# Optimization experiments

Measured on AMD Instinct MI355X. Metric: run time of the kernel, lower is better.

## Reference

```python
import jax, jax.numpy as jnp
from jax import lax
import numpy as np

B, TQ, T = 64, 2, 2048
HID, ENC, U, FILT, K = 1024, 512, 256, 32, 31


def setup_inputs() -> dict:
    key = jax.random.key(0)
    ks = jax.random.split(key, 12)
    def w(k, shape, fan_in):
        return jax.random.normal(k, shape, jnp.float32) / np.sqrt(fan_in)
    return {
        "query": jax.random.normal(ks[0], (B, TQ, HID), jnp.float32),
        "state": jax.random.uniform(ks[1], (B, T), jnp.float32),
        "memory": jax.random.normal(ks[2], (B, T, ENC), jnp.float32),
        "Wq": w(ks[3], (HID, U), HID), "bq": jnp.zeros((U,), jnp.float32),
        "Wm": w(ks[4], (ENC, U), ENC), "bm": jnp.zeros((U,), jnp.float32),
        "Wl": w(ks[5], (FILT, U), FILT), "bl": jnp.zeros((U,), jnp.float32),
        "conv_w": w(ks[6], (FILT, 1, K), K), "conv_b": jnp.zeros((FILT,), jnp.float32),
        "We": w(ks[7], (U, U), U), "be": jnp.zeros((U,), jnp.float32),
        "v_a": w(ks[8], (U,), U),
    }


def reference(query, state, memory, Wq, bq, Wm, bm, Wl, bl, conv_w, conv_b, We, be, v_a):
    # memory projection (done in `initialize` in the original): [B,T,U]
    mem_proj = jnp.einsum("bte,eu->btu", memory, Wm) + bm
    # query projection then slice timestep 1 -> [B,1,U]
    pq = (jnp.einsum("bqh,hu->bqu", query, Wq) + bq)[:, 1:2, :]
    # location features: 1-D conv over time of previous alignment, 'same' padding
    x = state[:, None, :]                                    # [B,1,T]
    f = lax.conv_general_dilated(x, conv_w, (1,), "SAME",
                                 dimension_numbers=("NCH", "OIH", "NCH"))
    f = f + conv_b[None, :, None]                            # [B,FILT,T]
    loc = jnp.einsum("bft,fu->btu", f, Wl) + bl              # [B,T,U]
    # additive energy with tanh, reduced against v_a -> [B,T]
    h = jnp.tanh(jnp.einsum("btu,uv->btv", pq + loc + mem_proj, We) + be)
    energy = jnp.einsum("btu,u->bt", h, v_a)
    # smoothing normalization: sigmoid / sum(sigmoid)
    s = jax.nn.sigmoid(energy)
    alignment = s / jnp.sum(s, axis=-1, keepdims=True)
    # cumulate_weights=True: accumulate onto previous alignment
    cum_alignment = state + alignment
    # context against projected memory: [B,1,U]
    context = jnp.einsum("bt,btu->bu", cum_alignment, mem_proj)[:, None, :]
    return context
```

## Files before the change

### kernel.cpp

```cpp
#include <hip/hip_runtime.h>
#include <hip/hip_bf16.h>
#include <math.h>

#define Bq 64
#define Tt 2048
#define TQn 2
#define HIDn 1024
#define ENCn 512
#define Un 256
#define FILTn 32
#define KKn 31

#define TTILE 32
#define NCHUNK (Tt / TTILE)
#define LDK 520

typedef short short8 __attribute__((ext_vector_type(8)));
typedef float f32x4  __attribute__((ext_vector_type(4)));
typedef unsigned short ushort_t;
typedef unsigned int   uint_t;

union S8 { short8 v; uint_t u[4]; };

__device__ __forceinline__ ushort_t f2b(float f) {
    union { float f; uint_t u; } x; x.f = f;
    uint_t r = x.u + 0x7fffu + ((x.u >> 16) & 1u);
    return (ushort_t)(r >> 16);
}
__device__ __forceinline__ uint_t cvt_pk(float lo, float hi) {
    union { __hip_bfloat162 h; uint_t u; } x;
    x.h = __float22bfloat162_rn(make_float2(lo, hi));
    return x.u;
}
__device__ __forceinline__ float b2f(uint_t u16) {
    union { uint_t i; float f; } x; x.i = u16 << 16;
    return x.f;
}
__device__ __forceinline__ float tanh_fast(float x) {
    const float e = __expf(2.0f * x);
    return 1.0f - 2.0f * __builtin_amdgcn_rcpf(e + 1.0f);
}

__global__ void k_prep1(const float* __restrict__ We, const float* __restrict__ Wm,
                        const float* __restrict__ Wl, const float* __restrict__ conv_w,
                        const float* __restrict__ bq, const float* __restrict__ bm,
                        const float* __restrict__ bl, const float* __restrict__ conv_b,
                        ushort_t* __restrict__ WmWeT, ushort_t* __restrict__ CWT,
                        float* __restrict__ cvec)
{
    const int blk = blockIdx.x;
    const int v = threadIdx.x;
    if (blk < 512) {
        const int e = blk;
        float a0 = 0.f, a1 = 0.f, a2 = 0.f, a3 = 0.f;
        #pragma unroll 4
        for (int u = 0; u < Un; u += 4) {
            a0 += Wm[(size_t)e * Un + u + 0] * We[(u + 0) * Un + v];
            a1 += Wm[(size_t)e * Un + u + 1] * We[(u + 1) * Un + v];
            a2 += Wm[(size_t)e * Un + u + 2] * We[(u + 2) * Un + v];
            a3 += Wm[(size_t)e * Un + u + 3] * We[(u + 3) * Un + v];
        }
        WmWeT[(size_t)v * ENCn + e] = f2b((a0 + a1) + (a2 + a3));
    } else if (blk < 516) {
        const int vc = (blk - 512) * 64;
        __shared__ float wlwe[FILTn * 64];
        for (int i = threadIdx.x; i < FILTn * 64; i += 256) {
            const int f = i >> 6, vv = i & 63;
            float a = 0.f;
            #pragma unroll 8
            for (int u = 0; u < Un; ++u) a += Wl[f * Un + u] * We[u * Un + vc + vv];
            wlwe[f * 64 + vv] = a;
        }
        __syncthreads();
        for (int i = threadIdx.x; i < 64 * 32; i += 256) {
            const int vv = i >> 5, k = i & 31;
            float a = 0.f;
            if (k < KKn) {
                #pragma unroll
                for (int f = 0; f < FILTn; ++f) a += conv_w[f * KKn + k] * wlwe[f * 64 + vv];
            }
            CWT[(size_t)(vc + vv) * 32 + k] = f2b(a);
        }
    } else {
        const int u = v;
        float a = bq[u] + bm[u] + bl[u];
        #pragma unroll
        for (int f = 0; f < FILTn; ++f) a += conv_b[f] * Wl[f * Un + u];
        cvec[u] = a;
    }
}

__global__ void k_g(const float* __restrict__ query, const float* __restrict__ Wq,
                    const float* __restrict__ cvec, float* __restrict__ g)
{
    const int b = blockIdx.x, hs = blockIdx.y * 128, u = threadIdx.x;
    const float* q = query + ((size_t)b * TQn + 1) * HIDn + hs;
    float a0 = 0.f, a1 = 0.f, a2 = 0.f, a3 = 0.f;
    #pragma unroll 4
    for (int h = 0; h < 128; h += 4) {
        a0 += q[h + 0] * Wq[(size_t)(hs + h + 0) * Un + u];
        a1 += q[h + 1] * Wq[(size_t)(hs + h + 1) * Un + u];
        a2 += q[h + 2] * Wq[(size_t)(hs + h + 2) * Un + u];
        a3 += q[h + 3] * Wq[(size_t)(hs + h + 3) * Un + u];
    }
    float acc = (a0 + a1) + (a2 + a3);
    if (blockIdx.y == 0) acc += cvec[u];
    atomicAdd(&g[b * Un + u], acc);
}

__global__ void k_zconst(const float* __restrict__ g, const float* __restrict__ We,
                         const float* __restrict__ be, float* __restrict__ zconst)
{
    const int b = blockIdx.x, us = blockIdx.y * 64, v = threadIdx.x;
    float a0 = 0.f, a1 = 0.f;
    #pragma unroll 4
    for (int u = us; u < us + 64; u += 2) {
        a0 += g[b * Un + u]     * We[(size_t)u * Un + v];
        a1 += g[b * Un + u + 1] * We[(size_t)(u + 1) * Un + v];
    }
    float acc = a0 + a1;
    if (blockIdx.y == 0) acc += be[v];
    atomicAdd(&zconst[b * Un + v], acc);
}

__global__ __launch_bounds__(256, 4) void attn_main(
    const float* __restrict__ memory, const float* __restrict__ state,
    const ushort_t* __restrict__ WmWeT, const ushort_t* __restrict__ CWT,
    const float* __restrict__ zconst, const float* __restrict__ v_a,
    float* __restrict__ zA, float* __restrict__ zS,
    float* __restrict__ zSsum, float* __restrict__ zStsum)
{
    const int blk = blockIdx.x;
    const int b  = blk >> 6;
    const int c  = blk & (NCHUNK - 1);
    const int t0 = c * TTILE;
    const int tid = threadIdx.x;

    __shared__ __align__(16) ushort_t mem_s[TTILE * LDK];
    __shared__ __align__(16) float sw_raw[80];
    __shared__ __align__(16) float ep_s[4][TTILE];
    __shared__ __align__(16) float s_s[TTILE];
    float* sw = sw_raw + 1;

    for (int i = tid; i < TTILE + 31; i += 256) {
        const int t = t0 - 15 + i;
        sw[i] = (t >= 0 && t < Tt) ? state[b * Tt + t] : 0.0f;
    }

    const int lane = tid & 63;
    const int w    = tid >> 6;
    const int lm   = lane & 15;
    const int lq   = lane >> 4;
    const int ncol0 = w * 64 + lm;

    const ushort_t* bp0 = WmWeT + (size_t)(ncol0 +  0) * ENCn + lq * 8;
    const ushort_t* bp1 = WmWeT + (size_t)(ncol0 + 16) * ENCn + lq * 8;
    const ushort_t* bp2 = WmWeT + (size_t)(ncol0 + 32) * ENCn + lq * 8;
    const ushort_t* bp3 = WmWeT + (size_t)(ncol0 + 48) * ENCn + lq * 8;

    short8 bbuf[2][4];
    bbuf[0][0] = *(const short8*)(bp0);      bbuf[0][1] = *(const short8*)(bp1);
    bbuf[0][2] = *(const short8*)(bp2);      bbuf[0][3] = *(const short8*)(bp3);
    bbuf[1][0] = *(const short8*)(bp0 + 32); bbuf[1][1] = *(const short8*)(bp1 + 32);
    bbuf[1][2] = *(const short8*)(bp2 + 32); bbuf[1][3] = *(const short8*)(bp3 + 32);

    const float4* memv4 = (const float4*)(memory + ((size_t)b * Tt + t0) * ENCn);
    #pragma unroll
    for (int i = 0; i < 8; ++i) {
        const int idx = i * 256 + tid;
        const int row = idx >> 6;
        const int cw8 = (idx & 63) << 3;
        const float4 m0 = memv4[2 * idx];
        const float4 m1 = memv4[2 * idx + 1];
        S8 v;
        v.u[0] = cvt_pk(m0.x, m0.y); v.u[1] = cvt_pk(m0.z, m0.w);
        v.u[2] = cvt_pk(m1.x, m1.y); v.u[3] = cvt_pk(m1.z, m1.w);
        *(short8*)&mem_s[row * LDK + cw8] = v.v;
    }

    f32x4 acc[2][4] = {};

    __syncthreads();

    const ushort_t* arow0 = &mem_s[(lm) * LDK + lq * 8];
    const ushort_t* arow1 = &mem_s[(16 + lm) * LDK + lq * 8];

    short8 a0c = *(const short8*)(arow0);
    short8 a1c = *(const short8*)(arow1);

    #pragma unroll
    for (int s = 0; s < 16; ++s) {
        const int sa = ((s + 1) & 15) * 32;
        const short8 a0n = *(const short8*)(arow0 + sa);
        const short8 a1n = *(const short8*)(arow1 + sa);
        acc[0][0] = __builtin_amdgcn_mfma_f32_16x16x32_bf16(a0c, bbuf[s & 1][0], acc[0][0], 0, 0, 0);
        acc[0][1] = __builtin_amdgcn_mfma_f32_16x16x32_bf16(a0c, bbuf[s & 1][1], acc[0][1], 0, 0, 0);
        acc[0][2] = __builtin_amdgcn_mfma_f32_16x16x32_bf16(a0c, bbuf[s & 1][2], acc[0][2], 0, 0, 0);
        acc[0][3] = __builtin_amdgcn_mfma_f32_16x16x32_bf16(a0c, bbuf[s & 1][3], acc[0][3], 0, 0, 0);
        acc[1][0] = __builtin_amdgcn_mfma_f32_16x16x32_bf16(a1c, bbuf[s & 1][0], acc[1][0], 0, 0, 0);
        acc[1][1] = __builtin_amdgcn_mfma_f32_16x16x32_bf16(a1c, bbuf[s & 1][1], acc[1][1], 0, 0, 0);
        acc[1][2] = __builtin_amdgcn_mfma_f32_16x16x32_bf16(a1c, bbuf[s & 1][2], acc[1][2], 0, 0, 0);
        acc[1][3] = __builtin_amdgcn_mfma_f32_16x16x32_bf16(a1c, bbuf[s & 1][3], acc[1][3], 0, 0, 0);
        const int sn = ((s + 2) & 15) * 32;
        bbuf[s & 1][0] = *(const short8*)(bp0 + sn);
        bbuf[s & 1][1] = *(const short8*)(bp1 + sn);
        bbuf[s & 1][2] = *(const short8*)(bp2 + sn);
        bbuf[s & 1][3] = *(const short8*)(bp3 + sn);
        a0c = a0n; a1c = a1n;
    }

    {
        S8 ca0, ca1;
        #pragma unroll
        for (int j = 0; j < 4; ++j) {
            const int base0 = lm + lq * 8 + 2 * j;
            ca0.u[j] = cvt_pk(sw[base0],      sw[base0 + 1]);
            ca1.u[j] = cvt_pk(sw[base0 + 16], sw[base0 + 17]);
        }
        const ushort_t* cp = CWT + (size_t)ncol0 * 32 + lq * 8;
        const short8 cb0 = *(const short8*)(cp);
        const short8 cb1 = *(const short8*)(cp + 16 * 32);
        const short8 cb2 = *(const short8*)(cp + 32 * 32);
        const short8 cb3 = *(const short8*)(cp + 48 * 32);
        acc[0][0] = __builtin_amdgcn_mfma_f32_16x16x32_bf16(ca0.v, cb0, acc[0][0], 0, 0, 0);
        acc[0][1] = __builtin_amdgcn_mfma_f32_16x16x32_bf16(ca0.v, cb1, acc[0][1], 0, 0, 0);
        acc[0][2] = __builtin_amdgcn_mfma_f32_16x16x32_bf16(ca0.v, cb2, acc[0][2], 0, 0, 0);
        acc[0][3] = __builtin_amdgcn_mfma_f32_16x16x32_bf16(ca0.v, cb3, acc[0][3], 0, 0, 0);
        acc[1][0] = __builtin_amdgcn_mfma_f32_16x16x32_bf16(ca1.v, cb0, acc[1][0], 0, 0, 0);
        acc[1][1] = __builtin_amdgcn_mfma_f32_16x16x32_bf16(ca1.v, cb1, acc[1][1], 0, 0, 0);
        acc[1][2] = __builtin_amdgcn_mfma_f32_16x16x32_bf16(ca1.v, cb2, acc[1][2], 0, 0, 0);
        acc[1][3] = __builtin_amdgcn_mfma_f32_16x16x32_bf16(ca1.v, cb3, acc[1][3], 0, 0, 0);
    }

    float zc[4], va[4];
    #pragma unroll
    for (int nbi = 0; nbi < 4; ++nbi) {
        const int col = ncol0 + nbi * 16;
        zc[nbi] = zconst[b * Un + col];
        va[nbi] = v_a[col];
    }
    #pragma unroll
    for (int mb = 0; mb < 2; ++mb) {
        #pragma unroll
        for (int r = 0; r < 4; ++r) {
            float ep = 0.f;
            #pragma unroll
            for (int nbi = 0; nbi < 4; ++nbi)
                ep += tanh_fast(acc[mb][nbi][r] + zc[nbi]) * va[nbi];
            ep += __shfl_xor(ep, 1, 64);
            ep += __shfl_xor(ep, 2, 64);
            ep += __shfl_xor(ep, 4, 64);
            ep += __shfl_xor(ep, 8, 64);
            if (lm == 0) ep_s[w][mb * 16 + lq * 4 + r] = ep;
        }
    }
    __syncthreads();

    if (tid < 64) {
        float s = 0.f, st = 0.f;
        if (tid < TTILE) {
            const float energy = ep_s[0][tid] + ep_s[1][tid] + ep_s[2][tid] + ep_s[3][tid];
            s = __builtin_amdgcn_rcpf(1.0f + __expf(-energy));
            s_s[tid] = s;
            st = sw[15 + tid];
        }
        float ssum = s, stsum = st;
        #pragma unroll
        for (int off = 32; off >= 1; off >>= 1) {
            ssum  += __shfl_xor(ssum,  off, 64);
            stsum += __shfl_xor(stsum, off, 64);
        }
        if (tid == 0) {
            atomicAdd(&zSsum[b], ssum);
            atomicAdd(&zStsum[b], stsum);
        }
    }
    __syncthreads();

    const int e0 = tid << 1;
    float aA0 = 0.f, aA1 = 0.f, aS0 = 0.f, aS1 = 0.f;
    #pragma unroll 2
    for (int r4 = 0; r4 < TTILE / 4; ++r4) {
        const float4 sv4 = *(const float4*)&s_s[r4 * 4];
        const float4 st4 = *(const float4*)&sw[15 + r4 * 4];
        const float sv[4] = {sv4.x, sv4.y, sv4.z, sv4.w};
        const float st[4] = {st4.x, st4.y, st4.z, st4.w};
        #pragma unroll
        for (int j = 0; j < 4; ++j) {
            const int r = r4 * 4 + j;
            const uint_t mm = *(const uint_t*)&mem_s[r * LDK + e0];
            const float m0 = b2f(mm & 0xffffu);
            const float m1 = b2f(mm >> 16);
            aA0 += st[j] * m0; aA1 += st[j] * m1;
            aS0 += sv[j] * m0; aS1 += sv[j] * m1;
        }
    }
    atomicAdd(&zA[b * ENCn + e0],     aA0);
    atomicAdd(&zA[b * ENCn + e0 + 1], aA1);
    atomicAdd(&zS[b * ENCn + e0],     aS0);
    atomicAdd(&zS[b * ENCn + e0 + 1], aS1);
}

__global__ void k_final(const float* __restrict__ zA, const float* __restrict__ zS,
                        const float* __restrict__ zSsum, const float* __restrict__ zStsum,
                        const float* __restrict__ Wm, const float* __restrict__ bm,
                        float* __restrict__ out)
{
    const int b = blockIdx.x, e0 = blockIdx.y * 128, u = threadIdx.x;
    const float inv = 1.0f / zSsum[b];
    float a0 = 0.f, a1 = 0.f;
    #pragma unroll 4
    for (int e = e0; e < e0 + 128; e += 2) {
        const float c0 = zA[b * ENCn + e]     + zS[b * ENCn + e]     * inv;
        const float c1 = zA[b * ENCn + e + 1] + zS[b * ENCn + e + 1] * inv;
        a0 += c0 * Wm[(size_t)e * Un + u];
        a1 += c1 * Wm[(size_t)(e + 1) * Un + u];
    }
    float acc = a0 + a1;
    if (blockIdx.y == 0) acc += bm[u] * (zStsum[b] + 1.0f);
    atomicAdd(&out[b * Un + u], acc);
}

extern "C" void kernel_launch(void* const* d_in, const int* in_sizes, int n_in,
                              void* d_out, int out_size, void* d_ws, size_t ws_size,
                              hipStream_t stream)
{
    const float* query  = (const float*)d_in[0];
    const float* state  = (const float*)d_in[1];
    const float* memory = (const float*)d_in[2];
    const float* Wq     = (const float*)d_in[3];
    const float* bq     = (const float*)d_in[4];
    const float* Wm     = (const float*)d_in[5];
    const float* bm     = (const float*)d_in[6];
    const float* Wl     = (const float*)d_in[7];
    const float* bl     = (const float*)d_in[8];
    const float* conv_w = (const float*)d_in[9];
    const float* conv_b = (const float*)d_in[10];
    const float* We     = (const float*)d_in[11];
    const float* be     = (const float*)d_in[12];
    const float* v_a    = (const float*)d_in[13];
    float* out = (float*)d_out;

    float* ws      = (float*)d_ws;
    float* zA      = ws;
    float* zS      = ws + 32768;
    float* zSsum   = ws + 65536;
    float* zStsum  = ws + 65600;
    float* g_      = ws + 65664;
    float* zconst  = ws + 82048;
    float* cvec    = ws + 98432;
    ushort_t* WmWeT = (ushort_t*)(ws + 98688);
    ushort_t* CWT   = (ushort_t*)(ws + 164224);

    hipMemsetAsync(ws, 0, 98432 * sizeof(float), stream);
    hipMemsetAsync(out, 0, (size_t)Bq * Un * sizeof(float), stream);

    hipLaunchKernelGGL(k_prep1, dim3(517), dim3(Un), 0, stream,
                       We, Wm, Wl, conv_w, bq, bm, bl, conv_b, WmWeT, CWT, cvec);
    hipLaunchKernelGGL(k_g, dim3(Bq, 8), dim3(Un), 0, stream, query, Wq, cvec, g_);
    hipLaunchKernelGGL(k_zconst, dim3(Bq, 4), dim3(Un), 0, stream, g_, We, be, zconst);
    hipLaunchKernelGGL(attn_main, dim3(Bq * NCHUNK), dim3(256), 0, stream,
                       memory, state, WmWeT, CWT, zconst, v_a, zA, zS, zSsum, zStsum);
    hipLaunchKernelGGL(k_final, dim3(Bq, 4), dim3(Un), 0, stream,
                       zA, zS, zSsum, zStsum, Wm, bm, out);
}
```

Measured before the change: 557.6 us.

## Process four time chunks per block with register prefetch and MFMA-packed weights

Each attn_main block now loops over four consecutive 32-step time tiles, prefetching the next tile of memory and state into registers while the current tile runs its MFMAs. This cuts the grid by four and amortizes atomics and setup. The WmWe and conv-weight matrices are stored in a fragment-packed layout so each lane reads contiguous 16-byte chunks. The cost is a large register prefetch buffer (launch bounds lowered to 3 blocks) and fewer blocks to spread across CUs.

```diff
diff --git a/kernel.cpp b/kernel.cpp
--- a/kernel.cpp
+++ b/kernel.cpp
@@ -13,6 +13,7 @@
 
 #define TTILE 32
 #define NCHUNK (Tt / TTILE)
+#define NCPB 4
 #define LDK 520
 
 typedef short short8 __attribute__((ext_vector_type(8)));
@@ -41,11 +42,17 @@
     return 1.0f - 2.0f * __builtin_amdgcn_rcpf(e + 1.0f);
 }
 
+__device__ __forceinline__ int bp_idx(int v, int k) {
+    const int seg = (k >> 5) * 16 + (v >> 6) * 4 + ((v >> 4) & 3);
+    const int ln  = ((k >> 3) & 3) * 16 + (v & 15);
+    return seg * 512 + ln * 8 + (k & 7);
+}
+
 __global__ void k_prep1(const float* __restrict__ We, const float* __restrict__ Wm,
                         const float* __restrict__ Wl, const float* __restrict__ conv_w,
                         const float* __restrict__ bq, const float* __restrict__ bm,
                         const float* __restrict__ bl, const float* __restrict__ conv_b,
-                        ushort_t* __restrict__ WmWeT, ushort_t* __restrict__ CWT,
+                        ushort_t* __restrict__ Bp, ushort_t* __restrict__ CWT,
                         float* __restrict__ cvec)
 {
     const int blk = blockIdx.x;
@@ -60,7 +67,7 @@
             a2 += Wm[(size_t)e * Un + u + 2] * We[(u + 2) * Un + v];
             a3 += Wm[(size_t)e * Un + u + 3] * We[(u + 3) * Un + v];
         }
-        WmWeT[(size_t)v * ENCn + e] = f2b((a0 + a1) + (a2 + a3));
+        Bp[bp_idx(v, e)] = f2b((a0 + a1) + (a2 + a3));
     } else if (blk < 516) {
         const int vc = (blk - 512) * 64;
         __shared__ float wlwe[FILTn * 64];
@@ -79,7 +86,7 @@
                 #pragma unroll
                 for (int f = 0; f < FILTn; ++f) a += conv_w[f * KKn + k] * wlwe[f * 64 + vv];
             }
-            CWT[(size_t)(vc + vv) * 32 + k] = f2b(a);
+            CWT[bp_idx(vc + vv, k)] = f2b(a);
         }
     } else {
         const int u = v;
@@ -123,17 +130,16 @@
     atomicAdd(&zconst[b * Un + v], acc);
 }
 
-__global__ __launch_bounds__(256, 4) void attn_main(
+__global__ __launch_bounds__(256, 3) void attn_main(
     const float* __restrict__ memory, const float* __restrict__ state,
-    const ushort_t* __restrict__ WmWeT, const ushort_t* __restrict__ CWT,
+    const ushort_t* __restrict__ Bp, const ushort_t* __restrict__ CWT,
     const float* __restrict__ zconst, const float* __restrict__ v_a,
     float* __restrict__ zA, float* __restrict__ zS,
     float* __restrict__ zSsum, float* __restrict__ zStsum)
 {
     const int blk = blockIdx.x;
-    const int b  = blk >> 6;
-    const int c  = blk & (NCHUNK - 1);
-    const int t0 = c * TTILE;
+    const int b  = blk >> 4;
+    const int cg = blk & 15;
     const int tid = threadIdx.x;
 
     __shared__ __align__(16) ushort_t mem_s[TTILE * LDK];
@@ -142,95 +148,17 @@
     __shared__ __align__(16) float s_s[TTILE];
     float* sw = sw_raw + 1;
 
-    for (int i = tid; i < TTILE + 31; i += 256) {
-        const int t = t0 - 15 + i;
-        sw[i] = (t >= 0 && t < Tt) ? state[b * Tt + t] : 0.0f;
-    }
-
     const int lane = tid & 63;
     const int w    = tid >> 6;
     const int lm   = lane & 15;
     const int lq   = lane >> 4;
     const int ncol0 = w * 64 + lm;
 
-    const ushort_t* bp0 = WmWeT + (size_t)(ncol0 +  0) * ENCn + lq * 8;
-    const ushort_t* bp1 = WmWeT + (size_t)(ncol0 + 16) * ENCn + lq * 8;
-    const ushort_t* bp2 = WmWeT + (size_t)(ncol0 + 32) * ENCn + lq * 8;
-    const ushort_t* bp3 = WmWeT + (size_t)(ncol0 + 48) * ENCn + lq * 8;
-
-    short8 bbuf[2][4];
-    bbuf[0][0] = *(const short8*)(bp0);      bbuf[0][1] = *(const short8*)(bp1);
-    bbuf[0][2] = *(const short8*)(bp2);      bbuf[0][3] = *(const short8*)(bp3);
-    bbuf[1][0] = *(const short8*)(bp0 + 32); bbuf[1][1] = *(const short8*)(bp1 + 32);
-    bbuf[1][2] = *(const short8*)(bp2 + 32); bbuf[1][3] = *(const short8*)(bp3 + 32);
-
-    const float4* memv4 = (const float4*)(memory + ((size_t)b * Tt + t0) * ENCn);
-    #pragma unroll
-    for (int i = 0; i < 8; ++i) {
-        const int idx = i * 256 + tid;
-        const int row = idx >> 6;
-        const int cw8 = (idx & 63) << 3;
-        const float4 m0 = memv4[2 * idx];
-        const float4 m1 = memv4[2 * idx + 1];
-        S8 v;
-        v.u[0] = cvt_pk(m0.x, m0.y); v.u[1] = cvt_pk(m0.z, m0.w);
-        v.u[2] = cvt_pk(m1.x, m1.y); v.u[3] = cvt_pk(m1.z, m1.w);
-        *(short8*)&mem_s[row * LDK + cw8] = v.v;
-    }
-
-    f32x4 acc[2][4] = {};
-
-    __syncthreads();
-
-    const ushort_t* arow0 = &mem_s[(lm) * LDK + lq * 8];
-    const ushort_t* arow1 = &mem_s[(16 + lm) * LDK + lq * 8];
-
-    short8 a0c = *(const short8*)(arow0);
-    short8 a1c = *(const short8*)(arow1);
-
-    #pragma unroll
-    for (int s = 0; s < 16; ++s) {
-        const int sa = ((s + 1) & 15) * 32;
-        const short8 a0n = *(const short8*)(arow0 + sa);
-        const short8 a1n = *(const short8*)(arow1 + sa);
-        acc[0][0] = __builtin_amdgcn_mfma_f32_16x16x32_bf16(a0c, bbuf[s & 1][0], acc[0][0], 0, 0, 0);
-        acc[0][1] = __builtin_amdgcn_mfma_f32_16x16x32_bf16(a0c, bbuf[s & 1][1], acc[0][1], 0, 0, 0);
-        acc[0][2] = __builtin_amdgcn_mfma_f32_16x16x32_bf16(a0c, bbuf[s & 1][2], acc[0][2], 0, 0, 0);
-        acc[0][3] = __builtin_amdgcn_mfma_f32_16x16x32_bf16(a0c, bbuf[s & 1][3], acc[0][3], 0, 0, 0);
-        acc[1][0] = __builtin_amdgcn_mfma_f32_16x16x32_bf16(a1c, bbuf[s & 1][0], acc[1][0], 0, 0, 0);
-        acc[1][1] = __builtin_amdgcn_mfma_f32_16x16x32_bf16(a1c, bbuf[s & 1][1], acc[1][1], 0, 0, 0);
-        acc[1][2] = __builtin_amdgcn_mfma_f32_16x16x32_bf16(a1c, bbuf[s & 1][2], acc[1][2], 0, 0, 0);
-        acc[1][3] = __builtin_amdgcn_mfma_f32_16x16x32_bf16(a1c, bbuf[s & 1][3], acc[1][3], 0, 0, 0);
-        const int sn = ((s + 2) & 15) * 32;
-        bbuf[s & 1][0] = *(const short8*)(bp0 + sn);
-        bbuf[s & 1][1] = *(const short8*)(bp1 + sn);
-        bbuf[s & 1][2] = *(const short8*)(bp2 + sn);
-        bbuf[s & 1][3] = *(const short8*)(bp3 + sn);
-        a0c = a0n; a1c = a1n;
-    }
-
-    {
-        S8 ca0, ca1;
-        #pragma unroll
-        for (int j = 0; j < 4; ++j) {
-            const int base0 = lm + lq * 8 + 2 * j;
-            ca0.u[j] = cvt_pk(sw[base0],      sw[base0 + 1]);
-            ca1.u[j] = cvt_pk(sw[base0 + 16], sw[base0 + 17]);
-        }
-        const ushort_t* cp = CWT + (size_t)ncol0 * 32 + lq * 8;
-        const short8 cb0 = *(const short8*)(cp);
-        const short8 cb1 = *(const short8*)(cp + 16 * 32);
-        const short8 cb2 = *(const short8*)(cp + 32 * 32);
-        const short8 cb3 = *(const short8*)(cp + 48 * 32);
-        acc[0][0] = __builtin_amdgcn_mfma_f32_16x16x32_bf16(ca0.v, cb0, acc[0][0], 0, 0, 0);
-        acc[0][1] = __builtin_amdgcn_mfma_f32_16x16x32_bf16(ca0.v, cb1, acc[0][1], 0, 0, 0);
-        acc[0][2] = __builtin_amdgcn_mfma_f32_16x16x32_bf16(ca0.v, cb2, acc[0][2], 0, 0, 0);
-        acc[0][3] = __builtin_amdgcn_mfma_f32_16x16x32_bf16(ca0.v, cb3, acc[0][3], 0, 0, 0);
-        acc[1][0] = __builtin_amdgcn_mfma_f32_16x16x32_bf16(ca1.v, cb0, acc[1][0], 0, 0, 0);
-        acc[1][1] = __builtin_amdgcn_mfma_f32_16x16x32_bf16(ca1.v, cb1, acc[1][1], 0, 0, 0);
-        acc[1][2] = __builtin_amdgcn_mfma_f32_16x16x32_bf16(ca1.v, cb2, acc[1][2], 0, 0, 0);
-        acc[1][3] = __builtin_amdgcn_mfma_f32_16x16x32_bf16(ca1.v, cb3, acc[1][3], 0, 0, 0);
-    }
+    const ushort_t* bp0 = Bp + (size_t)((w * 4 + 0) * 512 + lane * 8);
+    const ushort_t* bp1 = bp0 + 512;
+    const ushort_t* bp2 = bp0 + 1024;
+    const ushort_t* bp3 = bp0 + 1536;
+    const ushort_t* cp0 = CWT + (size_t)((w * 4 + 0) * 512 + lane * 8);
 
     float zc[4], va[4];
     #pragma unroll
@@ -239,61 +167,176 @@
         zc[nbi] = zconst[b * Un + col];
         va[nbi] = v_a[col];
     }
-    #pragma unroll
-    for (int mb = 0; mb < 2; ++mb) {
-        #pragma unroll
-        for (int r = 0; r < 4; ++r) {
-            float ep = 0.f;
-            #pragma unroll
-            for (int nbi = 0; nbi < 4; ++nbi)
-                ep += tanh_fast(acc[mb][nbi][r] + zc[nbi]) * va[nbi];
-            ep += __shfl_xor(ep, 1, 64);
-            ep += __shfl_xor(ep, 2, 64);
-            ep += __shfl_xor(ep, 4, 64);
-            ep += __shfl_xor(ep, 8, 64);
-            if (lm == 0) ep_s[w][mb * 16 + lq * 4 + r] = ep;
-        }
-    }
-    __syncthreads();
-
-    if (tid < 64) {
-        float s = 0.f, st = 0.f;
-        if (tid < TTILE) {
-            const float energy = ep_s[0][tid] + ep_s[1][tid] + ep_s[2][tid] + ep_s[3][tid];
-            s = __builtin_amdgcn_rcpf(1.0f + __expf(-energy));
-            s_s[tid] = s;
-            st = sw[15 + tid];
-        }
-        float ssum = s, stsum = st;
-        #pragma unroll
-        for (int off = 32; off >= 1; off >>= 1) {
-            ssum  += __shfl_xor(ssum,  off, 64);
-            stsum += __shfl_xor(stsum, off, 64);
-        }
-        if (tid == 0) {
-            atomicAdd(&zSsum[b], ssum);
-            atomicAdd(&zStsum[b], stsum);
-        }
-    }
-    __syncthreads();
 
     const int e0 = tid << 1;
     float aA0 = 0.f, aA1 = 0.f, aS0 = 0.f, aS1 = 0.f;
-    #pragma unroll 2
-    for (int r4 = 0; r4 < TTILE / 4; ++r4) {
-        const float4 sv4 = *(const float4*)&s_s[r4 * 4];
-        const float4 st4 = *(const float4*)&sw[15 + r4 * 4];
-        const float sv[4] = {sv4.x, sv4.y, sv4.z, sv4.w};
-        const float st[4] = {st4.x, st4.y, st4.z, st4.w};
+    float ssum_acc = 0.f, stsum_acc = 0.f;
+
+    float4 pf[16];
+    float  swv = 0.f;
+    {
+        const int t0 = (cg * NCPB) * TTILE;
+        const float4* memv4 = (const float4*)(memory + ((size_t)b * Tt + t0) * ENCn);
         #pragma unroll
-        for (int j = 0; j < 4; ++j) {
-            const int r = r4 * 4 + j;
-            const uint_t mm = *(const uint_t*)&mem_s[r * LDK + e0];
-            const float m0 = b2f(mm & 0xffffu);
-            const float m1 = b2f(mm >> 16);
-            aA0 += st[j] * m0; aA1 += st[j] * m1;
-            aS0 += sv[j] * m0; aS1 += sv[j] * m1;
-        }
+        for (int i = 0; i < 8; ++i) {
+            const int idx = i * 256 + tid;
+            pf[2 * i]     = memv4[2 * idx];
+            pf[2 * i + 1] = memv4[2 * idx + 1];
+        }
+        const int t = t0 - 15 + tid;
+        if (tid < 63 && t >= 0 && t < Tt) swv = state[b * Tt + t];
+    }
+
+    #pragma unroll 1
+    for (int cc = 0; cc < NCPB; ++cc) {
+        const int t0 = (cg * NCPB + cc) * TTILE;
+
+        if (cc) __syncthreads();
+
+        if (tid < 63) sw[tid] = swv;
+        #pragma unroll
+        for (int i = 0; i < 8; ++i) {
+            const int idx = i * 256 + tid;
+            const int row = idx >> 6;
+            const int cw8 = (idx & 63) << 3;
+            S8 v;
+            v.u[0] = cvt_pk(pf[2 * i].x,     pf[2 * i].y);
+            v.u[1] = cvt_pk(pf[2 * i].z,     pf[2 * i].w);
+            v.u[2] = cvt_pk(pf[2 * i + 1].x, pf[2 * i + 1].y);
+            v.u[3] = cvt_pk(pf[2 * i + 1].z, pf[2 * i + 1].w);
+            *(short8*)&mem_s[row * LDK + cw8] = v.v;
+        }
+        __syncthreads();
+
+        short8 bbuf[2][4];
+        bbuf[0][0] = *(const short8*)(bp0);
+        bbuf[0][1] = *(const short8*)(bp1);
+        bbuf[0][2] = *(const short8*)(bp2);
+        bbuf[0][3] = *(const short8*)(bp3);
+        bbuf[1][0] = *(const short8*)(bp0 + 8192);
+        bbuf[1][1] = *(const short8*)(bp1 + 8192);
+        bbuf[1][2] = *(const short8*)(bp2 + 8192);
+        bbuf[1][3] = *(const short8*)(bp3 + 8192);
+
+        if (cc < NCPB - 1) {
+            const float4* memn = (const float4*)(memory + ((size_t)b * Tt + t0 + TTILE) * ENCn);
+            #pragma unroll
+            for (int i = 0; i < 8; ++i) {
+                const int idx = i * 256 + tid;
+                pf[2 * i]     = memn[2 * idx];
+                pf[2 * i + 1] = memn[2 * idx + 1];
+            }
+            swv = 0.f;
+            const int t = t0 + TTILE - 15 + tid;
+            if (tid < 63 && t < Tt) swv = state[b * Tt + t];
+        }
+
+        f32x4 acc[2][4] = {};
+        const ushort_t* arow0 = &mem_s[(lm) * LDK + lq * 8];
+        const ushort_t* arow1 = &mem_s[(16 + lm) * LDK + lq * 8];
+        short8 a0c = *(const short8*)(arow0);
+        short8 a1c = *(const short8*)(arow1);
+
+        #pragma unroll
+        for (int s = 0; s < 16; ++s) {
+            const int sa = ((s + 1) & 15) * 32;
+            const short8 a0n = *(const short8*)(arow0 + sa);
+            const short8 a1n = *(const short8*)(arow1 + sa);
+            acc[0][0] = __builtin_amdgcn_mfma_f32_16x16x32_bf16(a0c, bbuf[s & 1][0], acc[0][0], 0, 0, 0);
+            acc[0][1] = __builtin_amdgcn_mfma_f32_16x16x32_bf16(a0c, bbuf[s & 1][1], acc[0][1], 0, 0, 0);
+            acc[0][2] = __builtin_amdgcn_mfma_f32_16x16x32_bf16(a0c, bbuf[s & 1][2], acc[0][2], 0, 0, 0);
+            acc[0][3] = __builtin_amdgcn_mfma_f32_16x16x32_bf16(a0c, bbuf[s & 1][3], acc[0][3], 0, 0, 0);
+            acc[1][0] = __builtin_amdgcn_mfma_f32_16x16x32_bf16(a1c, bbuf[s & 1][0], acc[1][0], 0, 0, 0);
+            acc[1][1] = __builtin_amdgcn_mfma_f32_16x16x32_bf16(a1c, bbuf[s & 1][1], acc[1][1], 0, 0, 0);
+            acc[1][2] = __builtin_amdgcn_mfma_f32_16x16x32_bf16(a1c, bbuf[s & 1][2], acc[1][2], 0, 0, 0);
+            acc[1][3] = __builtin_amdgcn_mfma_f32_16x16x32_bf16(a1c, bbuf[s & 1][3], acc[1][3], 0, 0, 0);
+            const int sn = ((s + 2) & 15) * 8192;
+            bbuf[s & 1][0] = *(const short8*)(bp0 + sn);
+            bbuf[s & 1][1] = *(const short8*)(bp1 + sn);
+            bbuf[s & 1][2] = *(const short8*)(bp2 + sn);
+            bbuf[s & 1][3] = *(const short8*)(bp3 + sn);
+            a0c = a0n; a1c = a1n;
+        }
+
+        {
+            S8 ca0, ca1;
+            #pragma unroll
+            for (int j = 0; j < 4; ++j) {
+                const int base0 = lm + lq * 8 + 2 * j;
+                ca0.u[j] = cvt_pk(sw[base0],      sw[base0 + 1]);
+                ca1.u[j] = cvt_pk(sw[base0 + 16], sw[base0 + 17]);
+            }
+            const short8 cb0 = *(const short8*)(cp0);
+            const short8 cb1 = *(const short8*)(cp0 + 512);
+            const short8 cb2 = *(const short8*)(cp0 + 1024);
+            const short8 cb3 = *(const short8*)(cp0 + 1536);
+            acc[0][0] = __builtin_amdgcn_mfma_f32_16x16x32_bf16(ca0.v, cb0, acc[0][0], 0, 0, 0);
+            acc[0][1] = __builtin_amdgcn_mfma_f32_16x16x32_bf16(ca0.v, cb1, acc[0][1], 0, 0, 0);
+            acc[0][2] = __builtin_amdgcn_mfma_f32_16x16x32_bf16(ca0.v, cb2, acc[0][2], 0, 0, 0);
+            acc[0][3] = __builtin_amdgcn_mfma_f32_16x16x32_bf16(ca0.v, cb3, acc[0][3], 0, 0, 0);
+            acc[1][0] = __builtin_amdgcn_mfma_f32_16x16x32_bf16(ca1.v, cb0, acc[1][0], 0, 0, 0);
+            acc[1][1] = __builtin_amdgcn_mfma_f32_16x16x32_bf16(ca1.v, cb1, acc[1][1], 0, 0, 0);
+            acc[1][2] = __builtin_amdgcn_mfma_f32_16x16x32_bf16(ca1.v, cb2, acc[1][2], 0, 0, 0);
+            acc[1][3] = __builtin_amdgcn_mfma_f32_16x16x32_bf16(ca1.v, cb3, acc[1][3], 0, 0, 0);
+        }
+
+        #pragma unroll
+        for (int mb = 0; mb < 2; ++mb) {
+            #pragma unroll
+            for (int r = 0; r < 4; ++r) {
+                float ep = 0.f;
+                #pragma unroll
+                for (int nbi = 0; nbi < 4; ++nbi)
+                    ep += tanh_fast(acc[mb][nbi][r] + zc[nbi]) * va[nbi];
+                ep += __shfl_xor(ep, 1, 64);
+                ep += __shfl_xor(ep, 2, 64);
+                ep += __shfl_xor(ep, 4, 64);
+                ep += __shfl_xor(ep, 8, 64);
+                if (lm == 0) ep_s[w][mb * 16 + lq * 4 + r] = ep;
+            }
+        }
+        __syncthreads();
+
+        if (tid < 64) {
+            float s = 0.f, st = 0.f;
+            if (tid < TTILE) {
+                const float energy = ep_s[0][tid] + ep_s[1][tid] + ep_s[2][tid] + ep_s[3][tid];
+                s = __builtin_amdgcn_rcpf(1.0f + __expf(-energy));
+                s_s[tid] = s;
+                st = sw[15 + tid];
+            }
+            float ssum = s, stsum = st;
+            #pragma unroll
+            for (int off = 32; off >= 1; off >>= 1) {
+                ssum  += __shfl_xor(ssum,  off, 64);
+                stsum += __shfl_xor(stsum, off, 64);
+            }
+            ssum_acc  += ssum;
+            stsum_acc += stsum;
+        }
+        __syncthreads();
+
+        #pragma unroll 2
+        for (int r4 = 0; r4 < TTILE / 4; ++r4) {
+            const float4 sv4 = *(const float4*)&s_s[r4 * 4];
+            const float4 st4 = *(const float4*)&sw[15 + r4 * 4];
+            const float sv[4] = {sv4.x, sv4.y, sv4.z, sv4.w};
+            const float st[4] = {st4.x, st4.y, st4.z, st4.w};
+            #pragma unroll
+            for (int j = 0; j < 4; ++j) {
+                const int r = r4 * 4 + j;
+                const uint_t mm = *(const uint_t*)&mem_s[r * LDK + e0];
+                const float m0 = b2f(mm & 0xffffu);
+                const float m1 = b2f(mm >> 16);
+                aA0 += st[j] * m0; aA1 += st[j] * m1;
+                aS0 += sv[j] * m0; aS1 += sv[j] * m1;
+            }
+        }
+    }
+
+    if (tid == 0) {
+        atomicAdd(&zSsum[b],  ssum_acc);
+        atomicAdd(&zStsum[b], stsum_acc);
     }
     atomicAdd(&zA[b * ENCn + e0],     aA0);
     atomicAdd(&zA[b * ENCn + e0 + 1], aA1);
@@ -349,18 +392,18 @@
     float* g_      = ws + 65664;
     float* zconst  = ws + 82048;
     float* cvec    = ws + 98432;
-    ushort_t* WmWeT = (ushort_t*)(ws + 98688);
+    ushort_t* Bp    = (ushort_t*)(ws + 98688);
     ushort_t* CWT   = (ushort_t*)(ws + 164224);
 
     hipMemsetAsync(ws, 0, 98432 * sizeof(float), stream);
     hipMemsetAsync(out, 0, (size_t)Bq * Un * sizeof(float), stream);
 
     hipLaunchKernelGGL(k_prep1, dim3(517), dim3(Un), 0, stream,
-                       We, Wm, Wl, conv_w, bq, bm, bl, conv_b, WmWeT, CWT, cvec);
+                       We, Wm, Wl, conv_w, bq, bm, bl, conv_b, Bp, CWT, cvec);
     hipLaunchKernelGGL(k_g, dim3(Bq, 8), dim3(Un), 0, stream, query, Wq, cvec, g_);
     hipLaunchKernelGGL(k_zconst, dim3(Bq, 4), dim3(Un), 0, stream, g_, We, be, zconst);
-    hipLaunchKernelGGL(attn_main, dim3(Bq * NCHUNK), dim3(256), 0, stream,
-                       memory, state, WmWeT, CWT, zconst, v_a, zA, zS, zSsum, zStsum);
+    hipLaunchKernelGGL(attn_main, dim3(Bq * NCHUNK / NCPB), dim3(256), 0, stream,
+                       memory, state, Bp, CWT, zconst, v_a, zA, zS, zSsum, zStsum);
     hipLaunchKernelGGL(k_final, dim3(Bq, 4), dim3(Un), 0, stream,
                        zA, zS, zSsum, zStsum, Wm, bm, out);
 }
```

Measured after the change: 726.5 us. 1.3x slower.

## Stream memory tile directly from global into MFMA fragments, drop LDS staging

Applied to the files above, without the earlier changes.

Removes the bf16 shared-memory copy of the 32x512 memory tile. Each wave now loads its A fragments straight from global fp32 memory and converts them in registers, prefetching one k-step ahead. The weight matrices are pre-permuted into a fragment-contiguous layout so each lane's B loads are coalesced. The final weighted reduction reads memory from global again in fp32 instead of from LDS. This cuts LDS use and may raise occupancy, but all four waves now read the same A rows redundantly from global/L2, and the memory tile is read twice.

```diff
diff --git a/kernel.cpp b/kernel.cpp
--- a/kernel.cpp
+++ b/kernel.cpp
@@ -13,7 +13,6 @@
 
 #define TTILE 32
 #define NCHUNK (Tt / TTILE)
-#define LDK 520
 
 typedef short short8 __attribute__((ext_vector_type(8)));
 typedef float f32x4  __attribute__((ext_vector_type(4)));
@@ -32,20 +31,22 @@
     x.h = __float22bfloat162_rn(make_float2(lo, hi));
     return x.u;
 }
-__device__ __forceinline__ float b2f(uint_t u16) {
-    union { uint_t i; float f; } x; x.i = u16 << 16;
-    return x.f;
-}
 __device__ __forceinline__ float tanh_fast(float x) {
     const float e = __expf(2.0f * x);
     return 1.0f - 2.0f * __builtin_amdgcn_rcpf(e + 1.0f);
+}
+
+__device__ __forceinline__ int bp_idx(int v, int k) {
+    const int seg = (k >> 5) * 16 + (v >> 6) * 4 + ((v >> 4) & 3);
+    const int ln  = ((k >> 3) & 3) * 16 + (v & 15);
+    return seg * 512 + ln * 8 + (k & 7);
 }
 
 __global__ void k_prep1(const float* __restrict__ We, const float* __restrict__ Wm,
                         const float* __restrict__ Wl, const float* __restrict__ conv_w,
                         const float* __restrict__ bq, const float* __restrict__ bm,
                         const float* __restrict__ bl, const float* __restrict__ conv_b,
-                        ushort_t* __restrict__ WmWeT, ushort_t* __restrict__ CWT,
+                        ushort_t* __restrict__ Bp, ushort_t* __restrict__ CWT,
                         float* __restrict__ cvec)
 {
     const int blk = blockIdx.x;
@@ -60,7 +61,7 @@
             a2 += Wm[(size_t)e * Un + u + 2] * We[(u + 2) * Un + v];
             a3 += Wm[(size_t)e * Un + u + 3] * We[(u + 3) * Un + v];
         }
-        WmWeT[(size_t)v * ENCn + e] = f2b((a0 + a1) + (a2 + a3));
+        Bp[bp_idx(v, e)] = f2b((a0 + a1) + (a2 + a3));
     } else if (blk < 516) {
         const int vc = (blk - 512) * 64;
         __shared__ float wlwe[FILTn * 64];
@@ -79,7 +80,7 @@
                 #pragma unroll
                 for (int f = 0; f < FILTn; ++f) a += conv_w[f * KKn + k] * wlwe[f * 64 + vv];
             }
-            CWT[(size_t)(vc + vv) * 32 + k] = f2b(a);
+            CWT[bp_idx(vc + vv, k)] = f2b(a);
         }
     } else {
         const int u = v;
@@ -125,7 +126,7 @@
 
 __global__ __launch_bounds__(256, 4) void attn_main(
     const float* __restrict__ memory, const float* __restrict__ state,
-    const ushort_t* __restrict__ WmWeT, const ushort_t* __restrict__ CWT,
+    const ushort_t* __restrict__ Bp, const ushort_t* __restrict__ CWT,
     const float* __restrict__ zconst, const float* __restrict__ v_a,
     float* __restrict__ zA, float* __restrict__ zS,
     float* __restrict__ zSsum, float* __restrict__ zStsum)
@@ -136,7 +137,6 @@
     const int t0 = c * TTILE;
     const int tid = threadIdx.x;
 
-    __shared__ __align__(16) ushort_t mem_s[TTILE * LDK];
     __shared__ __align__(16) float sw_raw[80];
     __shared__ __align__(16) float ep_s[4][TTILE];
     __shared__ __align__(16) float s_s[TTILE];
@@ -153,60 +153,64 @@
     const int lq   = lane >> 4;
     const int ncol0 = w * 64 + lm;
 
-    const ushort_t* bp0 = WmWeT + (size_t)(ncol0 +  0) * ENCn + lq * 8;
-    const ushort_t* bp1 = WmWeT + (size_t)(ncol0 + 16) * ENCn + lq * 8;
-    const ushort_t* bp2 = WmWeT + (size_t)(ncol0 + 32) * ENCn + lq * 8;
-    const ushort_t* bp3 = WmWeT + (size_t)(ncol0 + 48) * ENCn + lq * 8;
+    const ushort_t* bp0 = Bp + (size_t)(w * 4) * 512 + lane * 8;
+    const ushort_t* bp1 = bp0 + 512;
+    const ushort_t* bp2 = bp0 + 1024;
+    const ushort_t* bp3 = bp0 + 1536;
+    const ushort_t* cp0 = CWT + (size_t)(w * 4) * 512 + lane * 8;
 
     short8 bbuf[2][4];
-    bbuf[0][0] = *(const short8*)(bp0);      bbuf[0][1] = *(const short8*)(bp1);
-    bbuf[0][2] = *(const short8*)(bp2);      bbuf[0][3] = *(const short8*)(bp3);
-    bbuf[1][0] = *(const short8*)(bp0 + 32); bbuf[1][1] = *(const short8*)(bp1 + 32);
-    bbuf[1][2] = *(const short8*)(bp2 + 32); bbuf[1][3] = *(const short8*)(bp3 + 32);
-
-    const float4* memv4 = (const float4*)(memory + ((size_t)b * Tt + t0) * ENCn);
-    #pragma unroll
-    for (int i = 0; i < 8; ++i) {
-        const int idx = i * 256 + tid;
-        const int row = idx >> 6;
-        const int cw8 = (idx & 63) << 3;
-        const float4 m0 = memv4[2 * idx];
-        const float4 m1 = memv4[2 * idx + 1];
-        S8 v;
-        v.u[0] = cvt_pk(m0.x, m0.y); v.u[1] = cvt_pk(m0.z, m0.w);
-        v.u[2] = cvt_pk(m1.x, m1.y); v.u[3] = cvt_pk(m1.z, m1.w);
-        *(short8*)&mem_s[row * LDK + cw8] = v.v;
-    }
+    bbuf[0][0] = *(const short8*)(bp0);
+    bbuf[0][1] = *(const short8*)(bp1);
+    bbuf[0][2] = *(const short8*)(bp2);
+    bbuf[0][3] = *(const short8*)(bp3);
+    bbuf[1][0] = *(const short8*)(bp0 + 8192);
+    bbuf[1][1] = *(const short8*)(bp1 + 8192);
+    bbuf[1][2] = *(const short8*)(bp2 + 8192);
+    bbuf[1][3] = *(const short8*)(bp3 + 8192);
+
+    const float* gA0 = memory + ((size_t)b * Tt + t0 + lm) * ENCn + lq * 8;
+    const float* gA1 = gA0 + 16 * ENCn;
+
+    float4 n00 = *(const float4*)(gA0);
+    float4 n01 = *(const float4*)(gA0 + 4);
+    float4 n10 = *(const float4*)(gA1);
+    float4 n11 = *(const float4*)(gA1 + 4);
 
     f32x4 acc[2][4] = {};
 
     __syncthreads();
 
-    const ushort_t* arow0 = &mem_s[(lm) * LDK + lq * 8];
-    const ushort_t* arow1 = &mem_s[(16 + lm) * LDK + lq * 8];
-
-    short8 a0c = *(const short8*)(arow0);
-    short8 a1c = *(const short8*)(arow1);
+    S8 a0c, a1c;
+    a0c.u[0] = cvt_pk(n00.x, n00.y); a0c.u[1] = cvt_pk(n00.z, n00.w);
+    a0c.u[2] = cvt_pk(n01.x, n01.y); a0c.u[3] = cvt_pk(n01.z, n01.w);
+    a1c.u[0] = cvt_pk(n10.x, n10.y); a1c.u[1] = cvt_pk(n10.z, n10.w);
+    a1c.u[2] = cvt_pk(n11.x, n11.y); a1c.u[3] = cvt_pk(n11.z, n11.w);
 
     #pragma unroll
     for (int s = 0; s < 16; ++s) {
         const int sa = ((s + 1) & 15) * 32;
-        const short8 a0n = *(const short8*)(arow0 + sa);
-        const short8 a1n = *(const short8*)(arow1 + sa);
-        acc[0][0] = __builtin_amdgcn_mfma_f32_16x16x32_bf16(a0c, bbuf[s & 1][0], acc[0][0], 0, 0, 0);
-        acc[0][1] = __builtin_amdgcn_mfma_f32_16x16x32_bf16(a0c, bbuf[s & 1][1], acc[0][1], 0, 0, 0);
-        acc[0][2] = __builtin_amdgcn_mfma_f32_16x16x32_bf16(a0c, bbuf[s & 1][2], acc[0][2], 0, 0, 0);
-        acc[0][3] = __builtin_amdgcn_mfma_f32_16x16x32_bf16(a0c, bbuf[s & 1][3], acc[0][3], 0, 0, 0);
-        acc[1][0] = __builtin_amdgcn_mfma_f32_16x16x32_bf16(a1c, bbuf[s & 1][0], acc[1][0], 0, 0, 0);
-        acc[1][1] = __builtin_amdgcn_mfma_f32_16x16x32_bf16(a1c, bbuf[s & 1][1], acc[1][1], 0, 0, 0);
-        acc[1][2] = __builtin_amdgcn_mfma_f32_16x16x32_bf16(a1c, bbuf[s & 1][2], acc[1][2], 0, 0, 0);
-        acc[1][3] = __builtin_amdgcn_mfma_f32_16x16x32_bf16(a1c, bbuf[s & 1][3], acc[1][3], 0, 0, 0);
-        const int sn = ((s + 2) & 15) * 32;
+        n00 = *(const float4*)(gA0 + sa);
+        n01 = *(const float4*)(gA0 + sa + 4);
+        n10 = *(const float4*)(gA1 + sa);
+        n11 = *(const float4*)(gA1 + sa + 4);
+        acc[0][0] = __builtin_amdgcn_mfma_f32_16x16x32_bf16(a0c.v, bbuf[s & 1][0], acc[0][0], 0, 0, 0);
+        acc[0][1] = __builtin_amdgcn_mfma_f32_16x16x32_bf16(a0c.v, bbuf[s & 1][1], acc[0][1], 0, 0, 0);
+        acc[0][2] = __builtin_amdgcn_mfma_f32_16x16x32_bf16(a0c.v, bbuf[s & 1][2], acc[0][2], 0, 0, 0);
+        acc[0][3] = __builtin_amdgcn_mfma_f32_16x16x32_bf16(a0c.v, bbuf[s & 1][3], acc[0][3], 0, 0, 0);
+        acc[1][0] = __builtin_amdgcn_mfma_f32_16x16x32_bf16(a1c.v, bbuf[s & 1][0], acc[1][0], 0, 0, 0);
+        acc[1][1] = __builtin_amdgcn_mfma_f32_16x16x32_bf16(a1c.v, bbuf[s & 1][1], acc[1][1], 0, 0, 0);
+        acc[1][2] = __builtin_amdgcn_mfma_f32_16x16x32_bf16(a1c.v, bbuf[s & 1][2], acc[1][2], 0, 0, 0);
+        acc[1][3] = __builtin_amdgcn_mfma_f32_16x16x32_bf16(a1c.v, bbuf[s & 1][3], acc[1][3], 0, 0, 0);
+        const int sn = ((s + 2) & 15) * 8192;
         bbuf[s & 1][0] = *(const short8*)(bp0 + sn);
         bbuf[s & 1][1] = *(const short8*)(bp1 + sn);
         bbuf[s & 1][2] = *(const short8*)(bp2 + sn);
         bbuf[s & 1][3] = *(const short8*)(bp3 + sn);
-        a0c = a0n; a1c = a1n;
+        a0c.u[0] = cvt_pk(n00.x, n00.y); a0c.u[1] = cvt_pk(n00.z, n00.w);
+        a0c.u[2] = cvt_pk(n01.x, n01.y); a0c.u[3] = cvt_pk(n01.z, n01.w);
+        a1c.u[0] = cvt_pk(n10.x, n10.y); a1c.u[1] = cvt_pk(n10.z, n10.w);
+        a1c.u[2] = cvt_pk(n11.x, n11.y); a1c.u[3] = cvt_pk(n11.z, n11.w);
     }
 
     {
@@ -217,11 +221,10 @@
             ca0.u[j] = cvt_pk(sw[base0],      sw[base0 + 1]);
             ca1.u[j] = cvt_pk(sw[base0 + 16], sw[base0 + 17]);
         }
-        const ushort_t* cp = CWT + (size_t)ncol0 * 32 + lq * 8;
-        const short8 cb0 = *(const short8*)(cp);
-        const short8 cb1 = *(const short8*)(cp + 16 * 32);
-        const short8 cb2 = *(const short8*)(cp + 32 * 32);
-        const short8 cb3 = *(const short8*)(cp + 48 * 32);
+        const short8 cb0 = *(const short8*)(cp0);
+        const short8 cb1 = *(const short8*)(cp0 + 512);
+        const short8 cb2 = *(const short8*)(cp0 + 1024);
+        const short8 cb3 = *(const short8*)(cp0 + 1536);
         acc[0][0] = __builtin_amdgcn_mfma_f32_16x16x32_bf16(ca0.v, cb0, acc[0][0], 0, 0, 0);
         acc[0][1] = __builtin_amdgcn_mfma_f32_16x16x32_bf16(ca0.v, cb1, acc[0][1], 0, 0, 0);
         acc[0][2] = __builtin_amdgcn_mfma_f32_16x16x32_bf16(ca0.v, cb2, acc[0][2], 0, 0, 0);
@@ -278,22 +281,15 @@
     __syncthreads();
 
     const int e0 = tid << 1;
+    const float* gM = memory + ((size_t)b * Tt + t0) * ENCn + e0;
     float aA0 = 0.f, aA1 = 0.f, aS0 = 0.f, aS1 = 0.f;
-    #pragma unroll 2
-    for (int r4 = 0; r4 < TTILE / 4; ++r4) {
-        const float4 sv4 = *(const float4*)&s_s[r4 * 4];
-        const float4 st4 = *(const float4*)&sw[15 + r4 * 4];
-        const float sv[4] = {sv4.x, sv4.y, sv4.z, sv4.w};
-        const float st[4] = {st4.x, st4.y, st4.z, st4.w};
-        #pragma unroll
-        for (int j = 0; j < 4; ++j) {
-            const int r = r4 * 4 + j;
-            const uint_t mm = *(const uint_t*)&mem_s[r * LDK + e0];
-            const float m0 = b2f(mm & 0xffffu);
-            const float m1 = b2f(mm >> 16);
-            aA0 += st[j] * m0; aA1 += st[j] * m1;
-            aS0 += sv[j] * m0; aS1 += sv[j] * m1;
-        }
+    #pragma unroll 4
+    for (int r = 0; r < TTILE; ++r) {
+        const float2 mm = *(const float2*)(gM + (size_t)r * ENCn);
+        const float st = sw[15 + r];
+        const float sv = s_s[r];
+        aA0 += st * mm.x; aA1 += st * mm.y;
+        aS0 += sv * mm.x; aS1 += sv * mm.y;
     }
     atomicAdd(&zA[b * ENCn + e0],     aA0);
     atomicAdd(&zA[b * ENCn + e0 + 1], aA1);
@@ -349,18 +345,18 @@
     float* g_      = ws + 65664;
     float* zconst  = ws + 82048;
     float* cvec    = ws + 98432;
-    ushort_t* WmWeT = (ushort_t*)(ws + 98688);
+    ushort_t* Bp    = (ushort_t*)(ws + 98688);
     ushort_t* CWT   = (ushort_t*)(ws + 164224);
 
     hipMemsetAsync(ws, 0, 98432 * sizeof(float), stream);
     hipMemsetAsync(out, 0, (size_t)Bq * Un * sizeof(float), stream);
 
     hipLaunchKernelGGL(k_prep1, dim3(517), dim3(Un), 0, stream,
-                       We, Wm, Wl, conv_w, bq, bm, bl, conv_b, WmWeT, CWT, cvec);
+                       We, Wm, Wl, conv_w, bq, bm, bl, conv_b, Bp, CWT, cvec);
     hipLaunchKernelGGL(k_g, dim3(Bq, 8), dim3(Un), 0, stream, query, Wq, cvec, g_);
     hipLaunchKernelGGL(k_zconst, dim3(Bq, 4), dim3(Un), 0, stream, g_, We, be, zconst);
     hipLaunchKernelGGL(attn_main, dim3(Bq * NCHUNK), dim3(256), 0, stream,
-                       memory, state, WmWeT, CWT, zconst, v_a, zA, zS, zSsum, zStsum);
+                       memory, state, Bp, CWT, zconst, v_a, zA, zS, zSsum, zStsum);
     hipLaunchKernelGGL(k_final, dim3(Bq, 4), dim3(Un), 0, stream,
                        zA, zS, zSsum, zStsum, Wm, bm, out);
 }
```

Measured after the change: 608.4 us. +9.1%, slower.
